# Performance work log

Hardware: AMD Instinct MI355X
Metric: run time of the kernel (lower is better)

The kernel has to match this reference:

```python
import jax, jax.numpy as jnp
import numpy as np

B, S, D = 4, 2048, 1024
H = 16
HD = D // H


def setup_inputs() -> dict:
    key = jax.random.key(0)
    ks = jax.random.split(key, 5)
    scale = 0.02
    return {
        "x": jax.random.normal(ks[0], (B, S, D), dtype=jnp.float32),
        "wq": jax.random.normal(ks[1], (D, D), dtype=jnp.float32) * scale,
        "wk": jax.random.normal(ks[2], (D, D), dtype=jnp.float32) * scale,
        "wv": jax.random.normal(ks[3], (D, D), dtype=jnp.float32) * scale,
        "wo": jax.random.normal(ks[4], (D, D), dtype=jnp.float32) * scale,
    }


def reference(x, wq, wk, wv, wo):
    b, s, _ = x.shape
    # project and split heads: [b, h, s, hd]
    def proj(w):
        return jnp.einsum('bsd,de->bse', x, w).reshape(b, s, H, HD).transpose(0, 2, 1, 3)
    q, k, v = proj(wq), proj(wk), proj(wv)
    scores = jnp.einsum('bhqd,bhkd->bhqk', q, k)
    causal = jnp.tril(jnp.ones((s, s), dtype=bool))  # True = keep
    scores = jnp.where(causal, scores, -jnp.inf)
    attn = jax.nn.softmax(scores / jnp.sqrt(jnp.float32(HD)), axis=-1)
    ctx = jnp.einsum('bhqk,bhkd->bhqd', attn, v)
    ctx = ctx.transpose(0, 2, 1, 3).reshape(b, s, D)
    return jnp.einsum('bsd,de->bse', ctx, wo)
```

## Files before the change

kernel.cpp:

```cpp
#include <hip/hip_runtime.h>

#define S_LEN 2048
#define D_DIM 1024
#define NH    16
#define HD    64
#define BATCH 4
#define M_ROWS 8192

typedef __attribute__((ext_vector_type(8))) short bf16x8;
typedef __attribute__((ext_vector_type(4))) float f32x4;
typedef __attribute__((ext_vector_type(8))) unsigned short u16x8;

__device__ __forceinline__ unsigned short f2bf(float f) {
    unsigned u = __builtin_bit_cast(unsigned, f);
    u = (u + 0x7fffu + ((u >> 16) & 1u)) >> 16;
    return (unsigned short)u;
}
__device__ __forceinline__ unsigned pack2(float a, float b) {
    unsigned ua = __builtin_bit_cast(unsigned, a);
    unsigned ub = __builtin_bit_cast(unsigned, b);
    return ((ua + 0x8000u) >> 16) | ((ub + 0x8000u) & 0xffff0000u);
}

__device__ __forceinline__ void gload16(const void* g, void* l) {
    __builtin_amdgcn_global_load_lds((const __attribute__((address_space(1))) unsigned*)g,
                                     (__attribute__((address_space(3))) unsigned*)l,
                                     16, 0, 0);
}

template<int N> __device__ __forceinline__ void vmwait() {
    if constexpr (N == 0)      asm volatile("s_waitcnt vmcnt(0)" ::: "memory");
    else if constexpr (N == 3) asm volatile("s_waitcnt vmcnt(3)" ::: "memory");
    else if constexpr (N == 5) asm volatile("s_waitcnt vmcnt(5)" ::: "memory");
}

__global__ __launch_bounds__(256) void prep_k(const float* __restrict__ x,
                                              const float* __restrict__ w0, const float* __restrict__ w1,
                                              const float* __restrict__ w2, const float* __restrict__ w3,
                                              unsigned short* __restrict__ xbf,
                                              unsigned short* __restrict__ o0, unsigned short* __restrict__ o1,
                                              unsigned short* __restrict__ o2, unsigned short* __restrict__ o3) {
    __shared__ float sT[64][65];
    const int t = threadIdx.x;
    if (blockIdx.x < 4096) {
        size_t i = (size_t)blockIdx.x * 256 + t;
        const float4* xf = (const float4*)x;
        float4 a = xf[2 * i], b = xf[2 * i + 1];
        u16x8 v;
        v[0] = f2bf(a.x); v[1] = f2bf(a.y); v[2] = f2bf(a.z); v[3] = f2bf(a.w);
        v[4] = f2bf(b.x); v[5] = f2bf(b.y); v[6] = f2bf(b.z); v[7] = f2bf(b.w);
        *(u16x8*)(xbf + i * 8) = v;
        return;
    }
    const int wb = blockIdx.x - 4096;
    const int z = wb >> 8;
    const float* w; unsigned short* o;
    switch (z) {
        case 0: w = w0; o = o0; break;
        case 1: w = w1; o = o1; break;
        case 2: w = w2; o = o2; break;
        default: w = w3; o = o3; break;
    }
    const float sc = (z == 0) ? 0.18033688011112042f : 1.0f;
    const int n0 = (wb & 15) * 64, k0 = ((wb >> 4) & 15) * 64;
    const int r = t >> 4, cq = t & 15;
#pragma unroll
    for (int it = 0; it < 4; ++it) {
        int k = r + it * 16;
        float4 v = *(const float4*)&w[(size_t)(k0 + k) * D_DIM + n0 + cq * 4];
        sT[k][cq * 4 + 0] = v.x; sT[k][cq * 4 + 1] = v.y;
        sT[k][cq * 4 + 2] = v.z; sT[k][cq * 4 + 3] = v.w;
    }
    __syncthreads();
    const int n = t >> 2, ch = t & 3;
    union { unsigned short s[8]; uint4 v; } p0, p1;
#pragma unroll
    for (int j = 0; j < 8; ++j) p0.s[j] = f2bf(sT[ch * 16 + j][n] * sc);
#pragma unroll
    for (int j = 0; j < 8; ++j) p1.s[j] = f2bf(sT[ch * 16 + 8 + j][n] * sc);
    *(uint4*)&o[(size_t)(n0 + n) * D_DIM + k0 + ch * 16]     = p0.v;
    *(uint4*)&o[(size_t)(n0 + n) * D_DIM + k0 + ch * 16 + 8] = p1.v;
}

template<int MFRAG, int NFRAG, int AGLD, int BGLD>
__device__ __forceinline__ void gemm_core(const unsigned short* __restrict__ A,
                                          const unsigned short* __restrict__ Bt,
                                          unsigned short* __restrict__ sA,
                                          unsigned short* __restrict__ sB,
                                          int m0, int n0, int t,
                                          f32x4 (&acc)[MFRAG][NFRAG])
{
    constexpr int NGLD  = AGLD + BGLD;
    constexpr int ASLOT = AGLD * 4096;
    constexpr int BSLOT = BGLD * 4096;
    constexpr int NPH   = MFRAG / 2;

    const int lane = t & 63, wid = t >> 6;
    const int mm = lane & 15, quad = lane >> 4;
    const int wm = wid >> 2, wn = wid & 3;

    const int sr = t >> 2;
    const int sg = (t & 3) ^ ((sr >> 1) & 3);
    const unsigned short* asrc = A  + (size_t)(m0 + sr) * D_DIM + sg * 8;
    const unsigned short* bsrc = Bt + (size_t)(n0 + sr) * D_DIM + sg * 8;
    unsigned short* dA = sA + t * 8;
    unsigned short* dB = sB + t * 8;

    const int al = wm * (MFRAG * 16) + mm;
    const int bl = wn * (NFRAG * 16) + mm;
    const int xs = quad ^ ((mm >> 1) & 3);

#pragma unroll
    for (int pt = 0; pt < 2; ++pt) {
        const int ko = pt * 32;
#pragma unroll
        for (int i = 0; i < AGLD; ++i)
            gload16(asrc + (size_t)i * 128 * D_DIM + ko, dA + pt * ASLOT + i * 4096);
#pragma unroll
        for (int i = 0; i < BGLD; ++i)
            gload16(bsrc + (size_t)i * 128 * D_DIM + ko, dB + pt * BSLOT + i * 4096);
    }
    vmwait<NGLD>();
    __builtin_amdgcn_s_barrier();

    int sRead = 0, sWrite = 2;
    for (int T = 0; T < 32; ++T) {
        const int soA = sRead * ASLOT, soB = sRead * BSLOT;
        const int woA = sWrite * ASLOT, woB = sWrite * BSLOT;
        const int ko = (T + 2) * 32;
        const bool st = (T <= 29);

        bf16x8 bv[NFRAG];
#pragma unroll
        for (int p = 0; p < NPH; ++p) {
            if (p == 0) {
#pragma unroll
                for (int nf = 0; nf < NFRAG; ++nf)
                    bv[nf] = *(const bf16x8*)&sB[soB + (bl + nf * 16) * 32 + xs * 8];
            }
            bf16x8 af0 = *(const bf16x8*)&sA[soA + (al + (2 * p) * 16) * 32 + xs * 8];
            bf16x8 af1 = *(const bf16x8*)&sA[soA + (al + (2 * p + 1) * 16) * 32 + xs * 8];

            if (st) {
                if (p == 0) {
#pragma unroll
                    for (int i = 0; i < AGLD; ++i)
                        gload16(asrc + (size_t)i * 128 * D_DIM + ko, dA + woA + i * 4096);
                } else {
#pragma unroll
                    for (int i = 0; i < BGLD; ++i)
                        if ((i % (NPH - 1)) == p - 1)
                            gload16(bsrc + (size_t)i * 128 * D_DIM + ko, dB + woB + i * 4096);
                }
            }

            __builtin_amdgcn_s_barrier();
            asm volatile("s_waitcnt lgkmcnt(0)" ::: "memory");
            __builtin_amdgcn_s_setprio(1);
#pragma unroll
            for (int nf = 0; nf < NFRAG; ++nf) {
                acc[2 * p][nf]     = __builtin_amdgcn_mfma_f32_16x16x32_bf16(af0, bv[nf], acc[2 * p][nf], 0, 0, 0);
                acc[2 * p + 1][nf] = __builtin_amdgcn_mfma_f32_16x16x32_bf16(af1, bv[nf], acc[2 * p + 1][nf], 0, 0, 0);
            }
            __builtin_amdgcn_s_setprio(0);
            if (p == NPH - 1) {
                if (T <= 29)      vmwait<NGLD>();
                else if (T == 30) vmwait<0>();
            }
            __builtin_amdgcn_s_barrier();
        }

        sRead  = (sRead  == 2) ? 0 : sRead + 1;
        sWrite = (sWrite == 2) ? 0 : sWrite + 1;
    }
}

__global__ __launch_bounds__(512, 2) void gemmqkv_k(const unsigned short* __restrict__ A,
                                                    const unsigned short* __restrict__ Bt,
                                                    unsigned short* __restrict__ qb,
                                                    unsigned short* __restrict__ kb,
                                                    unsigned short* __restrict__ vt)
{
    __shared__ unsigned short sA[3 * 2 * 4096];
    __shared__ unsigned short sB[3 * 3 * 4096];
    const int t = threadIdx.x;
    const int bid = blockIdx.x;
    const int wg = (bid & 7) * 32 + (bid >> 3);
    const int mt = wg >> 3, nt = wg & 7;
    const int m0 = mt * 256, n0 = nt * 384;

    f32x4 acc[8][6];
#pragma unroll
    for (int i = 0; i < 8; ++i)
#pragma unroll
        for (int j = 0; j < 6; ++j) acc[i][j] = (f32x4){0.f, 0.f, 0.f, 0.f};

    gemm_core<8, 6, 2, 3>(A, Bt, sA, sB, m0, n0, t, acc);

    const int lane = t & 63, wid = t >> 6;
    const int mm = lane & 15, quad = lane >> 4;
    const int wm = wid >> 2, wn = wid & 3;

#pragma unroll
    for (int nf = 0; nf < 6; ++nf) {
        const int c0 = n0 + wn * 96 + nf * 16;
        const int widx = c0 >> 10, nl0 = c0 & 1023;
        if (widx == 2) {
            const int h = nl0 >> 6, hd = (nl0 & 63) + mm;
#pragma unroll
            for (int mf = 0; mf < 8; ++mf) {
                int rglob = m0 + wm * 128 + mf * 16 + quad * 4;
                int bb = rglob >> 11, ss = rglob & (S_LEN - 1);
                union { unsigned short s[4]; unsigned long long ll; } pk;
#pragma unroll
                for (int r = 0; r < 4; ++r) pk.s[r] = f2bf(acc[mf][nf][r]);
                *(unsigned long long*)&vt[((size_t)(bb * NH + h) * HD + hd) * S_LEN + ss] = pk.ll;
            }
        } else {
            unsigned short* outp = widx ? kb : qb;
#pragma unroll
            for (int mf = 0; mf < 8; ++mf)
#pragma unroll
                for (int r = 0; r < 4; ++r)
                    outp[(size_t)(m0 + wm * 128 + mf * 16 + quad * 4 + r) * D_DIM +
                         nl0 + mm] = f2bf(acc[mf][nf][r]);
        }
    }
}

__global__ __launch_bounds__(512, 2) void gemmo_k(const unsigned short* __restrict__ A,
                                                  const unsigned short* __restrict__ Bt,
                                                  float* __restrict__ C)
{
    __shared__ unsigned short sA[3 * 4096];
    __shared__ unsigned short sB[3 * 2 * 4096];
    const int t = threadIdx.x;
    const int bid = blockIdx.x;
    const int wg = (bid & 7) * 32 + (bid >> 3);
    const int mt = wg >> 2, nt = wg & 3;
    const int m0 = mt * 128, n0 = nt * 256;

    f32x4 acc[4][4];
#pragma unroll
    for (int i = 0; i < 4; ++i)
#pragma unroll
        for (int j = 0; j < 4; ++j) acc[i][j] = (f32x4){0.f, 0.f, 0.f, 0.f};

    gemm_core<4, 4, 1, 2>(A, Bt, sA, sB, m0, n0, t, acc);

    const int lane = t & 63, wid = t >> 6;
    const int mm = lane & 15, quad = lane >> 4;
    const int wm = wid >> 2, wn = wid & 3;

#pragma unroll
    for (int mf = 0; mf < 4; ++mf)
#pragma unroll
        for (int nf = 0; nf < 4; ++nf)
#pragma unroll
            for (int r = 0; r < 4; ++r)
                C[(size_t)(m0 + wm * 64 + mf * 16 + quad * 4 + r) * D_DIM +
                  n0 + wn * 64 + nf * 16 + mm] = acc[mf][nf][r];
}

__global__ __launch_bounds__(512, 4) void attn_k(const unsigned short* __restrict__ Q,
                                                 const unsigned short* __restrict__ K,
                                                 const unsigned short* __restrict__ Vt,
                                                 unsigned short* __restrict__ ctx)
{
    __shared__ unsigned short sK [2][64 * 64];
    __shared__ unsigned short sVT[2][64 * 64];
    __shared__ unsigned short sP [128 * 64];
    const int t = threadIdx.x;
    const int lane = t & 63, w = t >> 6;
    const int mm = lane & 15, quad = lane >> 4;
    const int pair = blockIdx.x, bh = blockIdx.y;
    const int b = bh >> 4, hh = bh & 15;
    const size_t rowbase = (size_t)b * S_LEN;
    const int coff = hh * HD;
    const unsigned short* Vh = Vt + (size_t)bh * HD * S_LEN;

    const int sc_ = t >> 3, sj = t & 7;
    const int sgk = sj ^ (sc_ & 7);

    u16x8 onesu;
#pragma unroll
    for (int j = 0; j < 8; ++j) onesu[j] = 0x3F80;
    const bf16x8 ones = __builtin_bit_cast(bf16x8, onesu);

    for (int sidx = 0; sidx < 2; ++sidx) {
        const int qt = sidx ? (15 - pair) : pair;
        const int q0 = qt * 128;

        bf16x8 qf[2];
#pragma unroll
        for (int kk = 0; kk < 2; ++kk)
            qf[kk] = *(const bf16x8*)(Q + (rowbase + q0 + w * 16 + mm) * D_DIM
                                        + coff + kk * 32 + quad * 8);
        f32x4 o[4], lacc;
        lacc = (f32x4){0.f, 0.f, 0.f, 0.f};
#pragma unroll
        for (int hf = 0; hf < 4; ++hf) o[hf] = (f32x4){0.f, 0.f, 0.f, 0.f};

        const int nkt = 2 * qt + 2;
        const int qr = q0 + w * 16 + mm;
        const int qrmax = q0 + w * 16 + 15;
        const int m = w * 16 + mm;

        gload16(K  + (rowbase + sc_) * D_DIM + coff + sgk * 8, (void*)&sK[0][t * 8]);
        gload16(Vh + (size_t)sc_ * S_LEN + sgk * 8,            (void*)&sVT[0][t * 8]);

        for (int kt = 0; kt < nkt; ++kt) {
            const int buf = kt & 1;
            __syncthreads();
            if (kt + 1 < nkt) {
                const int k1 = (kt + 1) * 64;
                gload16(K  + (rowbase + k1 + sc_) * D_DIM + coff + sgk * 8,
                        (void*)&sK[1 - buf][t * 8]);
                gload16(Vh + (size_t)sc_ * S_LEN + k1 + sgk * 8,
                        (void*)&sVT[1 - buf][t * 8]);
            }
            const int k0 = kt * 64;
            if (k0 > qrmax) continue;

            f32x4 sacc[4];
#pragma unroll
            for (int kf = 0; kf < 4; ++kf) sacc[kf] = (f32x4){0.f, 0.f, 0.f, 0.f};
#pragma unroll
            for (int kk = 0; kk < 2; ++kk) {
                bf16x8 ak[4];
#pragma unroll
                for (int kf = 0; kf < 4; ++kf) {
                    int key = kf * 16 + mm;
                    int slot = (kk * 4 + quad) ^ (key & 7);
                    ak[kf] = *(const bf16x8*)&sK[buf][key * 64 + slot * 8];
                }
#pragma unroll
                for (int kf = 0; kf < 4; ++kf)
                    sacc[kf] = __builtin_amdgcn_mfma_f32_16x16x32_bf16(ak[kf], qf[kk], sacc[kf], 0, 0, 0);
            }

            const bool needmask = (k0 + 63) > (q0 + w * 16);
#pragma unroll
            for (int kf = 0; kf < 4; ++kf) {
                float p[4];
#pragma unroll
                for (int r = 0; r < 4; ++r) {
                    p[r] = __builtin_amdgcn_exp2f(sacc[kf][r]);
                    if (needmask && (k0 + kf * 16 + quad * 4 + r) > qr) p[r] = 0.f;
                }
                unsigned lo = pack2(p[0], p[1]), hi = pack2(p[2], p[3]);
                int slot = (kf * 2 + (quad >> 1)) ^ (m & 7);
                *(unsigned long long*)&sP[m * 64 + slot * 8 + (quad & 1) * 4] =
                    ((unsigned long long)hi << 32) | lo;
            }

#pragma unroll
            for (int kk = 0; kk < 2; ++kk) {
                bf16x8 pf, vf[4];
                {
                    int slot = (kk * 4 + quad) ^ (m & 7);
                    pf = *(const bf16x8*)&sP[m * 64 + slot * 8];
                }
#pragma unroll
                for (int hf = 0; hf < 4; ++hf) {
                    int hd = hf * 16 + mm;
                    int slot = (kk * 4 + quad) ^ (hd & 7);
                    vf[hf] = *(const bf16x8*)&sVT[buf][hd * 64 + slot * 8];
                }
                lacc = __builtin_amdgcn_mfma_f32_16x16x32_bf16(pf, ones, lacc, 0, 0, 0);
#pragma unroll
                for (int hf = 0; hf < 4; ++hf)
                    o[hf] = __builtin_amdgcn_mfma_f32_16x16x32_bf16(pf, vf[hf], o[hf], 0, 0, 0);
            }
        }
        __syncthreads();

#pragma unroll
        for (int r = 0; r < 4; ++r) {
            float inv = 1.f / lacc[r];
            int row = q0 + w * 16 + quad * 4 + r;
#pragma unroll
            for (int hf = 0; hf < 4; ++hf)
                ctx[(rowbase + row) * D_DIM + coff + hf * 16 + mm] = f2bf(o[hf][r] * inv);
        }
    }
}

extern "C" void kernel_launch(void* const* d_in, const int* in_sizes, int n_in,
                              void* d_out, int out_size, void* d_ws, size_t ws_size,
                              hipStream_t stream)
{
    const float* x  = (const float*)d_in[0];
    const float* wq = (const float*)d_in[1];
    const float* wk = (const float*)d_in[2];
    const float* wv = (const float*)d_in[3];
    const float* wo = (const float*)d_in[4];

    const size_t XE = (size_t)M_ROWS * D_DIM;
    const size_t WE = (size_t)D_DIM * D_DIM;
    unsigned short* ws  = (unsigned short*)d_ws;
    unsigned short* xbf = ws;
    unsigned short* wt0 = xbf + XE;
    unsigned short* wt1 = wt0 + WE;
    unsigned short* wt2 = wt1 + WE;
    unsigned short* wt3 = wt2 + WE;
    unsigned short* qb  = wt3 + WE;
    unsigned short* kb  = qb + XE;
    unsigned short* vt  = kb + XE;
    unsigned short* cb  = vt + XE;

    prep_k<<<dim3(4096 + 1024), 256, 0, stream>>>(x, wq, wk, wv, wo,
                                                  xbf, wt0, wt1, wt2, wt3);

    gemmqkv_k<<<dim3(256), 512, 0, stream>>>(xbf, wt0, qb, kb, vt);

    attn_k<<<dim3(8, BATCH * NH), 512, 0, stream>>>(qb, kb, vt, cb);

    gemmo_k<<<dim3(256), 512, 0, stream>>>(cb, wt3, (float*)d_out);
}
```

Measured before the change: 244.0 us.

## Rewrite attention with 32x32 MFMA and register-resident P via permlane swap

Switches the attention kernel from 16x16x32 to 32x32x16 bf16 MFMA with 4 waves each owning 32 query rows, computing S transposed so P stays in registers. P is converted with v_cvt_pk_bf16_f32 and rearranged via v_permlane32_swap, removing the shared-memory P round trip. The grid is flattened and remapped for locality, and s_setprio brackets the MFMA sections. The cost is fewer threads per block, higher register pressure, and a lower occupancy hint.

```diff
diff --git a/kernel.cpp b/kernel.cpp
--- a/kernel.cpp
+++ b/kernel.cpp
@@ -9,6 +9,7 @@
 
 typedef __attribute__((ext_vector_type(8))) short bf16x8;
 typedef __attribute__((ext_vector_type(4))) float f32x4;
+typedef __attribute__((ext_vector_type(16))) float f32x16;
 typedef __attribute__((ext_vector_type(8))) unsigned short u16x8;
 
 __device__ __forceinline__ unsigned short f2bf(float f) {
@@ -16,11 +17,6 @@
     u = (u + 0x7fffu + ((u >> 16) & 1u)) >> 16;
     return (unsigned short)u;
 }
-__device__ __forceinline__ unsigned pack2(float a, float b) {
-    unsigned ua = __builtin_bit_cast(unsigned, a);
-    unsigned ub = __builtin_bit_cast(unsigned, b);
-    return ((ua + 0x8000u) >> 16) | ((ub + 0x8000u) & 0xffff0000u);
-}
 
 __device__ __forceinline__ void gload16(const void* g, void* l) {
     __builtin_amdgcn_global_load_lds((const __attribute__((address_space(1))) unsigned*)g,
@@ -32,6 +28,15 @@
     if constexpr (N == 0)      asm volatile("s_waitcnt vmcnt(0)" ::: "memory");
     else if constexpr (N == 3) asm volatile("s_waitcnt vmcnt(3)" ::: "memory");
     else if constexpr (N == 5) asm volatile("s_waitcnt vmcnt(5)" ::: "memory");
+}
+
+__device__ __forceinline__ unsigned cvtpk_bf16(float lo, float hi) {
+    unsigned r;
+    asm("v_cvt_pk_bf16_f32 %0, %1, %2" : "=v"(r) : "v"(lo), "v"(hi));
+    return r;
+}
+__device__ __forceinline__ void pl32swap(unsigned &a, unsigned &b) {
+    asm("v_permlane32_swap_b32 %0, %1" : "+v"(a), "+v"(b));
 }
 
 __global__ __launch_bounds__(256) void prep_k(const float* __restrict__ x,
@@ -262,25 +267,28 @@
                   n0 + wn * 64 + nf * 16 + mm] = acc[mf][nf][r];
 }
 
-__global__ __launch_bounds__(512, 4) void attn_k(const unsigned short* __restrict__ Q,
+__global__ __launch_bounds__(256, 2) void attn_k(const unsigned short* __restrict__ Q,
                                                  const unsigned short* __restrict__ K,
                                                  const unsigned short* __restrict__ Vt,
                                                  unsigned short* __restrict__ ctx)
 {
     __shared__ unsigned short sK [2][64 * 64];
     __shared__ unsigned short sVT[2][64 * 64];
-    __shared__ unsigned short sP [128 * 64];
     const int t = threadIdx.x;
     const int lane = t & 63, w = t >> 6;
-    const int mm = lane & 15, quad = lane >> 4;
-    const int pair = blockIdx.x, bh = blockIdx.y;
+    const int m5 = lane & 31, h = lane >> 5;
+    const int m7 = m5 & 7;
+    const int bid = blockIdx.x;
+    const int ii = bid >> 3;
+    const int bh = (bid & 7) * 8 + (ii >> 3);
+    const int pair = ii & 7;
     const int b = bh >> 4, hh = bh & 15;
     const size_t rowbase = (size_t)b * S_LEN;
     const int coff = hh * HD;
     const unsigned short* Vh = Vt + (size_t)bh * HD * S_LEN;
 
-    const int sc_ = t >> 3, sj = t & 7;
-    const int sgk = sj ^ (sc_ & 7);
+    const int sc = t >> 3, sj = t & 7;
+    const int sg = (sj ^ (sc & 7)) * 8;
 
     u16x8 onesu;
 #pragma unroll
@@ -290,98 +298,105 @@
     for (int sidx = 0; sidx < 2; ++sidx) {
         const int qt = sidx ? (15 - pair) : pair;
         const int q0 = qt * 128;
-
-        bf16x8 qf[2];
-#pragma unroll
-        for (int kk = 0; kk < 2; ++kk)
-            qf[kk] = *(const bf16x8*)(Q + (rowbase + q0 + w * 16 + mm) * D_DIM
-                                        + coff + kk * 32 + quad * 8);
-        f32x4 o[4], lacc;
-        lacc = (f32x4){0.f, 0.f, 0.f, 0.f};
-#pragma unroll
-        for (int hf = 0; hf < 4; ++hf) o[hf] = (f32x4){0.f, 0.f, 0.f, 0.f};
+        const int qrw = q0 + w * 32;
+        const int qr  = qrw + m5;
+
+        bf16x8 qf[4];
+#pragma unroll
+        for (int s = 0; s < 4; ++s)
+            qf[s] = *(const bf16x8*)(Q + (rowbase + qr) * D_DIM + coff + s * 16 + h * 8);
+
+        f32x16 o0, o1, l16;
+#pragma unroll
+        for (int r = 0; r < 16; ++r) { o0[r] = 0.f; o1[r] = 0.f; l16[r] = 0.f; }
 
         const int nkt = 2 * qt + 2;
-        const int qr = q0 + w * 16 + mm;
-        const int qrmax = q0 + w * 16 + 15;
-        const int m = w * 16 + mm;
-
-        gload16(K  + (rowbase + sc_) * D_DIM + coff + sgk * 8, (void*)&sK[0][t * 8]);
-        gload16(Vh + (size_t)sc_ * S_LEN + sgk * 8,            (void*)&sVT[0][t * 8]);
+
+        gload16(K  + (rowbase + sc) * D_DIM + coff + sg,      (void*)&sK[0][t * 8]);
+        gload16(K  + (rowbase + sc + 32) * D_DIM + coff + sg, (void*)&sK[0][2048 + t * 8]);
+        gload16(Vh + (size_t)sc * S_LEN + sg,                 (void*)&sVT[0][t * 8]);
+        gload16(Vh + (size_t)(sc + 32) * S_LEN + sg,          (void*)&sVT[0][2048 + t * 8]);
 
         for (int kt = 0; kt < nkt; ++kt) {
             const int buf = kt & 1;
             __syncthreads();
             if (kt + 1 < nkt) {
                 const int k1 = (kt + 1) * 64;
-                gload16(K  + (rowbase + k1 + sc_) * D_DIM + coff + sgk * 8,
-                        (void*)&sK[1 - buf][t * 8]);
-                gload16(Vh + (size_t)sc_ * S_LEN + k1 + sgk * 8,
-                        (void*)&sVT[1 - buf][t * 8]);
+                gload16(K  + (rowbase + k1 + sc) * D_DIM + coff + sg,      (void*)&sK[1 - buf][t * 8]);
+                gload16(K  + (rowbase + k1 + sc + 32) * D_DIM + coff + sg, (void*)&sK[1 - buf][2048 + t * 8]);
+                gload16(Vh + (size_t)sc * S_LEN + k1 + sg,                 (void*)&sVT[1 - buf][t * 8]);
+                gload16(Vh + (size_t)(sc + 32) * S_LEN + k1 + sg,          (void*)&sVT[1 - buf][2048 + t * 8]);
             }
             const int k0 = kt * 64;
-            if (k0 > qrmax) continue;
-
-            f32x4 sacc[4];
-#pragma unroll
-            for (int kf = 0; kf < 4; ++kf) sacc[kf] = (f32x4){0.f, 0.f, 0.f, 0.f};
-#pragma unroll
-            for (int kk = 0; kk < 2; ++kk) {
-                bf16x8 ak[4];
-#pragma unroll
-                for (int kf = 0; kf < 4; ++kf) {
-                    int key = kf * 16 + mm;
-                    int slot = (kk * 4 + quad) ^ (key & 7);
-                    ak[kf] = *(const bf16x8*)&sK[buf][key * 64 + slot * 8];
+            if (k0 > qrw + 31) continue;
+
+            f32x16 s0, s1;
+#pragma unroll
+            for (int r = 0; r < 16; ++r) { s0[r] = 0.f; s1[r] = 0.f; }
+            __builtin_amdgcn_s_setprio(1);
+#pragma unroll
+            for (int s = 0; s < 4; ++s) {
+                const int sl = ((2 * s + h) ^ m7) * 8;
+                bf16x8 ak0 = *(const bf16x8*)&sK[buf][m5 * 64 + sl];
+                bf16x8 ak1 = *(const bf16x8*)&sK[buf][(32 + m5) * 64 + sl];
+                s0 = __builtin_amdgcn_mfma_f32_32x32x16_bf16(ak0, qf[s], s0, 0, 0, 0);
+                s1 = __builtin_amdgcn_mfma_f32_32x32x16_bf16(ak1, qf[s], s1, 0, 0, 0);
+            }
+            __builtin_amdgcn_s_setprio(0);
+
+            const bool needmask = (k0 + 63) > qrw;
+            bf16x8 pb[4];
+#pragma unroll
+            for (int kf = 0; kf < 2; ++kf) {
+                unsigned pw[8];
+#pragma unroll
+                for (int j = 0; j < 8; ++j) {
+                    float plo = __builtin_amdgcn_exp2f(kf ? s1[2 * j] : s0[2 * j]);
+                    float phi = __builtin_amdgcn_exp2f(kf ? s1[2 * j + 1] : s0[2 * j + 1]);
+                    if (needmask) {
+                        const int kb_ = k0 + kf * 32 + 4 * h;
+                        const int r0 = 2 * j, r1 = 2 * j + 1;
+                        if (kb_ + (r0 & 3) + 8 * (r0 >> 2) > qr) plo = 0.f;
+                        if (kb_ + (r1 & 3) + 8 * (r1 >> 2) > qr) phi = 0.f;
+                    }
+                    pw[j] = cvtpk_bf16(plo, phi);
                 }
-#pragma unroll
-                for (int kf = 0; kf < 4; ++kf)
-                    sacc[kf] = __builtin_amdgcn_mfma_f32_16x16x32_bf16(ak[kf], qf[kk], sacc[kf], 0, 0, 0);
-            }
-
-            const bool needmask = (k0 + 63) > (q0 + w * 16);
-#pragma unroll
-            for (int kf = 0; kf < 4; ++kf) {
-                float p[4];
-#pragma unroll
-                for (int r = 0; r < 4; ++r) {
-                    p[r] = __builtin_amdgcn_exp2f(sacc[kf][r]);
-                    if (needmask && (k0 + kf * 16 + quad * 4 + r) > qr) p[r] = 0.f;
-                }
-                unsigned lo = pack2(p[0], p[1]), hi = pack2(p[2], p[3]);
-                int slot = (kf * 2 + (quad >> 1)) ^ (m & 7);
-                *(unsigned long long*)&sP[m * 64 + slot * 8 + (quad & 1) * 4] =
-                    ((unsigned long long)hi << 32) | lo;
-            }
-
-#pragma unroll
-            for (int kk = 0; kk < 2; ++kk) {
-                bf16x8 pf, vf[4];
-                {
-                    int slot = (kk * 4 + quad) ^ (m & 7);
-                    pf = *(const bf16x8*)&sP[m * 64 + slot * 8];
-                }
-#pragma unroll
-                for (int hf = 0; hf < 4; ++hf) {
-                    int hd = hf * 16 + mm;
-                    int slot = (kk * 4 + quad) ^ (hd & 7);
-                    vf[hf] = *(const bf16x8*)&sVT[buf][hd * 64 + slot * 8];
-                }
-                lacc = __builtin_amdgcn_mfma_f32_16x16x32_bf16(pf, ones, lacc, 0, 0, 0);
-#pragma unroll
-                for (int hf = 0; hf < 4; ++hf)
-                    o[hf] = __builtin_amdgcn_mfma_f32_16x16x32_bf16(pf, vf[hf], o[hf], 0, 0, 0);
-            }
+                pl32swap(pw[0], pw[2]);
+                pl32swap(pw[1], pw[3]);
+                pl32swap(pw[4], pw[6]);
+                pl32swap(pw[5], pw[7]);
+                union { unsigned u[4]; bf16x8 v; } f0, f1;
+                f0.u[0] = pw[0]; f0.u[1] = pw[1]; f0.u[2] = pw[2]; f0.u[3] = pw[3];
+                f1.u[0] = pw[4]; f1.u[1] = pw[5]; f1.u[2] = pw[6]; f1.u[3] = pw[7];
+                pb[kf * 2 + 0] = f0.v;
+                pb[kf * 2 + 1] = f1.v;
+            }
+
+            __builtin_amdgcn_s_setprio(1);
+#pragma unroll
+            for (int s = 0; s < 4; ++s) {
+                const int sl = ((2 * s + h) ^ m7) * 8;
+                bf16x8 vf0 = *(const bf16x8*)&sVT[buf][m5 * 64 + sl];
+                bf16x8 vf1 = *(const bf16x8*)&sVT[buf][(32 + m5) * 64 + sl];
+                l16 = __builtin_amdgcn_mfma_f32_32x32x16_bf16(ones, pb[s], l16, 0, 0, 0);
+                o0  = __builtin_amdgcn_mfma_f32_32x32x16_bf16(vf0,  pb[s], o0, 0, 0, 0);
+                o1  = __builtin_amdgcn_mfma_f32_32x32x16_bf16(vf1,  pb[s], o1, 0, 0, 0);
+            }
+            __builtin_amdgcn_s_setprio(0);
         }
         __syncthreads();
 
-#pragma unroll
-        for (int r = 0; r < 4; ++r) {
-            float inv = 1.f / lacc[r];
-            int row = q0 + w * 16 + quad * 4 + r;
-#pragma unroll
-            for (int hf = 0; hf < 4; ++hf)
-                ctx[(rowbase + row) * D_DIM + coff + hf * 16 + mm] = f2bf(o[hf][r] * inv);
+        const float linv = 1.f / l16[0];
+#pragma unroll
+        for (int hf = 0; hf < 2; ++hf) {
+#pragma unroll
+            for (int rg = 0; rg < 4; ++rg) {
+                union { unsigned short s4[4]; unsigned long long ll; } pk4;
+#pragma unroll
+                for (int r = 0; r < 4; ++r)
+                    pk4.s4[r] = f2bf((hf ? o1[rg * 4 + r] : o0[rg * 4 + r]) * linv);
+                *(unsigned long long*)&ctx[(rowbase + qr) * D_DIM + coff + hf * 32 + 8 * rg + 4 * h] = pk4.ll;
+            }
         }
     }
 }
@@ -414,7 +429,7 @@
 
     gemmqkv_k<<<dim3(256), 512, 0, stream>>>(xbf, wt0, qb, kb, vt);
 
-    attn_k<<<dim3(8, BATCH * NH), 512, 0, stream>>>(qb, kb, vt, cb);
+    attn_k<<<dim3(512), 256, 0, stream>>>(qb, kb, vt, cb);
 
     gemmo_k<<<dim3(256), 512, 0, stream>>>(cb, wt3, (float*)d_out);
 }
```

New measurement: 236.4 us. 3.1% less time.
